# Kernel tuning notes

Measured on AMD Instinct MI355X. Metric: run time of the kernel, lower is better.

Reference implementation:

```python
import jax, jax.numpy as jnp
import numpy as np

B, T = 8, 4096
EMBED_DIM = 128
ENGRAM_EMBED_DIM = 64
VOCAB_SIZES = [4096, 4096]
MAX_NGRAM = 3
NUM_HEADS = 2
N_STREAMS = 4
KERNEL = 4
TOTAL_NGRAMS = len(VOCAB_SIZES) * NUM_HEADS          # 4
INPUT_DIM = TOTAL_NGRAMS * ENGRAM_EMBED_DIM          # 256
TOTAL_SLOTS = sum(VOCAB_SIZES) * NUM_HEADS           # 16384


def setup_inputs() -> dict:
    key = jax.random.key(0)
    ks = jax.random.split(key, 10)
    x = jax.random.normal(ks[0], (B, T, N_STREAMS, EMBED_DIM), dtype=jnp.float32)
    input_ids = jax.random.randint(ks[1], (B, T), 0, 50257, dtype=jnp.int32)
    multipliers = jax.random.randint(ks[2], (MAX_NGRAM - 1, NUM_HEADS, MAX_NGRAM), 1, 10000, dtype=jnp.int32)
    embedding = jax.random.normal(ks[3], (TOTAL_SLOTS, ENGRAM_EMBED_DIM), dtype=jnp.float32) * 0.02
    val_W = jax.random.normal(ks[4], (EMBED_DIM, INPUT_DIM), dtype=jnp.float32) * 0.05
    val_b = jnp.zeros((EMBED_DIM,), jnp.float32)
    key_W = jax.random.normal(ks[5], (N_STREAMS, EMBED_DIM, INPUT_DIM), dtype=jnp.float32) * 0.05
    key_b = jnp.zeros((N_STREAMS, EMBED_DIM), jnp.float32)
    normq_w = jnp.ones((N_STREAMS, EMBED_DIM), jnp.float32)
    normk_w = jnp.ones((N_STREAMS, EMBED_DIM), jnp.float32)
    conv_w = jax.random.normal(ks[6], (N_STREAMS * EMBED_DIM, 1, KERNEL), dtype=jnp.float32) * 0.1
    convnorm_w = jnp.ones((N_STREAMS, EMBED_DIM), jnp.float32)
    return {"x": x, "input_ids": input_ids, "multipliers": multipliers,
            "embedding": embedding, "val_W": val_W, "val_b": val_b,
            "key_W": key_W, "key_b": key_b, "normq_w": normq_w,
            "normk_w": normk_w, "conv_w": conv_w, "convnorm_w": convnorm_w}


def rmsnorm(v, w):
    # torch nn.RMSNorm default eps = finfo(dtype).eps
    eps = jnp.finfo(v.dtype).eps
    return v * jax.lax.rsqrt(jnp.mean(v * v, axis=-1, keepdims=True) + eps) * w


def hash_ids_fn(input_ids, multipliers):
    padded = jnp.pad(input_ids, ((0, 0), (MAX_NGRAM - 1, 0)))            # [B, T+2]
    windows = jnp.stack([padded[:, i:i + T] for i in range(MAX_NGRAM)], axis=-1)  # [B,T,3]
    hashes = []
    for n_idx in range(MAX_NGRAM - 1):
        ngram_len = n_idx + 2
        grams = windows[:, :, MAX_NGRAM - ngram_len:]                    # [B,T,L]
        mults = multipliers[n_idx, :, :ngram_len]                        # [H,L]
        mixed = grams[:, :, None, :] * mults[None, None, :, :]           # [B,T,H,L]
        h = mixed[..., 0]
        for k in range(1, ngram_len):
            h = jnp.bitwise_xor(h, mixed[..., k])
        hashes.append(h % VOCAB_SIZES[n_idx])                            # [B,T,H]
    return jnp.concatenate(hashes, axis=2)                               # [B,T,4]


def engram_forward(x, input_ids, multipliers, embedding, val_W, val_b,
                   key_W, key_b, normq_w, normk_w, conv_w, convnorm_w):
    hids = hash_ids_fn(input_ids, multipliers)
    offsets = jnp.cumsum(jnp.array([0] + [v for v in VOCAB_SIZES for _ in range(NUM_HEADS)], jnp.int32))[:-1]
    ids = hids + offsets                                                 # [B,T,4]
    emb = embedding[ids].reshape(B, T, INPUT_DIM)                        # [B,T,256]
    v_base = emb @ val_W.T + val_b                                       # [B,T,128]
    k = rmsnorm(jnp.einsum('bte,gde->btgd', emb, key_W) + key_b, normk_w)  # [B,T,G,D]
    q = rmsnorm(x, normq_w)                                              # [B,T,G,D]
    score = jnp.sum(q * k, axis=-1, keepdims=True) / (EMBED_DIM ** 0.5)
    gates = jax.nn.sigmoid(score)                                        # [B,T,G,1]
    v_gated = v_base[:, :, None, :] * gates                              # [B,T,G,D]
    # ShortConv: per-chunk RMSNorm -> causal depthwise conv -> SiLU
    xn = rmsnorm(v_gated, convnorm_w).reshape(B, T, N_STREAMS * EMBED_DIM)
    x_bct = jnp.transpose(xn, (0, 2, 1))                                 # [B,C,T]
    x_bct = jnp.pad(x_bct, ((0, 0), (0, 0), (KERNEL - 1, 0)))            # causal left pad
    y_bct = jax.lax.conv_general_dilated(
        x_bct, conv_w, window_strides=(1,), padding='VALID',
        dimension_numbers=('NCH', 'OIH', 'NCH'),
        feature_group_count=N_STREAMS * EMBED_DIM)                       # [B,C,T]
    y = jax.nn.silu(y_bct)
    y = jnp.transpose(y, (0, 2, 1)).reshape(B, T, N_STREAMS, EMBED_DIM)
    return v_gated + y


def reference(x, input_ids, multipliers, embedding, val_W, val_b,
              key_W, key_b, normq_w, normk_w, conv_w, convnorm_w):
    return engram_forward(x, input_ids, multipliers, embedding, val_W, val_b,
                          key_W, key_b, normq_w, normk_w, conv_w, convnorm_w)
```

## Files before the change

### kernel.cpp

```cpp
#include <hip/hip_runtime.h>
#include <math.h>

#define EPS 1.1920928955078125e-07f

typedef __attribute__((ext_vector_type(8)))  short short8;
typedef __attribute__((ext_vector_type(4)))  short short4v;
typedef __attribute__((ext_vector_type(16))) float floatx16;

__device__ __forceinline__ float4 ld4(const float* __restrict__ p) { return *(const float4* __restrict__)p; }
__device__ __forceinline__ void   st4(float* __restrict__ p, float4 v) { *(float4* __restrict__)p = v; }

__device__ __forceinline__ unsigned short f2bf(float f) {
    union { float f; unsigned u; } v; v.f = f;
    unsigned r = v.u + 0x7fffu + ((v.u >> 16) & 1u);
    return (unsigned short)(r >> 16);
}

__global__ __launch_bounds__(256) void build_pack(const float* __restrict__ val_W,
                                                  const float* __restrict__ key_W,
                                                  const float* __restrict__ emb,
                                                  unsigned short* __restrict__ WbF,
                                                  unsigned short* __restrict__ ebf)
{
    int bid = blockIdx.x;
    if (bid < 80) {
        int idx  = bid * 256 + threadIdx.x;
        int lane = idx & 63;
        int ks   = (idx >> 6) & 15;
        int nt   = idx >> 10;
        int n = (nt << 5) + (lane & 31);
        int k = (ks << 4) + ((lane >> 5) << 3);
        const float* src = (n < 512) ? key_W + (size_t)n * 256 + k
                                     : val_W + (size_t)(n - 512) * 256 + k;
        float4 v0 = ld4(src), v1 = ld4(src + 4);
        unsigned short o[8] = { f2bf(v0.x), f2bf(v0.y), f2bf(v0.z), f2bf(v0.w),
                                f2bf(v1.x), f2bf(v1.y), f2bf(v1.z), f2bf(v1.w) };
        unsigned short* dst = WbF + (size_t)idx * 8;
        *(short4v*)dst       = *(short4v*)&o[0];
        *(short4v*)(dst + 4) = *(short4v*)&o[4];
    } else {
        int idx = (bid - 80) * 256 + threadIdx.x;
        const float* src = emb + ((size_t)idx << 3);
        float4 v0 = ld4(src), v1 = ld4(src + 4);
        unsigned short o[8] = { f2bf(v0.x), f2bf(v0.y), f2bf(v0.z), f2bf(v0.w),
                                f2bf(v1.x), f2bf(v1.y), f2bf(v1.z), f2bf(v1.w) };
        unsigned short* dst = ebf + ((size_t)idx << 3);
        *(short4v*)dst       = *(short4v*)&o[0];
        *(short4v*)(dst + 4) = *(short4v*)&o[4];
    }
}

__global__ __launch_bounds__(256, 4) void engram_gemm(
    const float* __restrict__ x,
    const int*   __restrict__ input_ids,
    const int*   __restrict__ mult,
    const unsigned short* __restrict__ ebf,
    const float* __restrict__ val_b,
    const float* __restrict__ key_b,
    const float* __restrict__ normq_w,
    const float* __restrict__ normk_w,
    const unsigned short* __restrict__ WbF,
    float* __restrict__ v_base,
    float* __restrict__ Gbuf,
    float* __restrict__ S2buf)
{
    __shared__ int   sids[32][4];
    __shared__ short A[32 * 260];
    __shared__ float D[32 * 130];

    const int tid  = threadIdx.x;
    const int tok0 = blockIdx.x << 5;

    if (tid < 32) {
        int token = tok0 + tid;
        int b = token >> 12, t = token & 4095;
        const int* row = input_ids + (b << 12);
        unsigned g2 = (unsigned)row[t];
        unsigned g1 = (t >= 1) ? (unsigned)row[t - 1] : 0u;
        unsigned g0 = (t >= 2) ? (unsigned)row[t - 2] : 0u;
        sids[tid][0] = (int)(((g1 * (unsigned)mult[0]) ^ (g2 * (unsigned)mult[1])) & 4095u);
        sids[tid][1] = (int)((((g1 * (unsigned)mult[3]) ^ (g2 * (unsigned)mult[4])) & 4095u) + 4096u);
        sids[tid][2] = (int)((((g0 * (unsigned)mult[6]) ^ (g1 * (unsigned)mult[7]) ^ (g2 * (unsigned)mult[8])) & 4095u) + 8192u);
        sids[tid][3] = (int)((((g0 * (unsigned)mult[9]) ^ (g1 * (unsigned)mult[10]) ^ (g2 * (unsigned)mult[11])) & 4095u) + 12288u);
    }
    __syncthreads();

    #pragma unroll
    for (int it = 0; it < 4; ++it) {
        int f = (it << 8) + tid;
        int token = f >> 5, ch = f & 31;
        const unsigned short* src = ebf + ((size_t)sids[token][ch >> 3] << 6) + ((ch & 7) << 3);
        short4v lo = *(const short4v*)src;
        short4v hi = *(const short4v*)(src + 4);
        short* dst = A + token * 260 + (ch << 3);
        *(short4v*)dst       = lo;
        *(short4v*)(dst + 4) = hi;
    }
    __syncthreads();

    const int lane = tid & 63;
    const int wv   = tid >> 6;
    const int half = lane >> 5;
    const int mrow = lane & 31;

    const short*  Ap = A + mrow * 260 + (half << 3);
    const float4* Bf = (const float4*)WbF + lane;

    const int ty = tid >> 4, tx = tid & 15;
    const int tx8 = tx << 3;
    const int colw = (wv << 5) + mrow;
    const int rb   = half << 2;

    for (int s = 0; s < 4; ++s) {
        const float* xp0 = x + ((((size_t)(tok0 + (ty << 1))     << 2) + s) << 7) + tx8;
        const float* xp1 = x + ((((size_t)(tok0 + (ty << 1) + 1) << 2) + s) << 7) + tx8;
        float4 xa0 = ld4(xp0), xb0 = ld4(xp0 + 4);
        float4 xa1 = ld4(xp1), xb1 = ld4(xp1 + 4);

        floatx16 acc;
        #pragma unroll
        for (int r = 0; r < 16; ++r) acc[r] = 0.f;
        const int nt = (s << 2) + wv;
        const float4* bp = Bf + ((size_t)(nt << 4) << 6);
        #pragma unroll 4
        for (int ks = 0; ks < 16; ++ks) {
            short4v al = *(const short4v*)(Ap + (ks << 4));
            short4v ah = *(const short4v*)(Ap + (ks << 4) + 4);
            short8 a = { al[0], al[1], al[2], al[3], ah[0], ah[1], ah[2], ah[3] };
            union { float4 f; short8 s8; } ub;
            ub.f = bp[(size_t)ks << 6];
            acc = __builtin_amdgcn_mfma_f32_32x32x16_bf16(a, ub.s8, acc, 0, 0, 0);
        }

        __syncthreads();
        #pragma unroll
        for (int r = 0; r < 16; ++r) {
            int row = (r & 3) + ((r >> 2) << 3) + rb;
            D[row * 130 + colw] = acc[r];
        }
        __syncthreads();

        const float* kbp = key_b   + (s << 7) + tx8;
        const float* nqp = normq_w + (s << 7) + tx8;
        const float* nkp = normk_w + (s << 7) + tx8;
        float4 kba = ld4(kbp), kbb = ld4(kbp + 4);
        float4 nqa = ld4(nqp), nqb = ld4(nqp + 4);
        float4 nka = ld4(nkp), nkb = ld4(nkp + 4);
        float kb[8] = {kba.x, kba.y, kba.z, kba.w, kbb.x, kbb.y, kbb.z, kbb.w};
        float nq[8] = {nqa.x, nqa.y, nqa.z, nqa.w, nqb.x, nqb.y, nqb.z, nqb.w};
        float nk[8] = {nka.x, nka.y, nka.z, nka.w, nkb.x, nkb.y, nkb.z, nkb.w};
        #pragma unroll
        for (int jj = 0; jj < 2; ++jj) {
            int t_loc = (ty << 1) + jj;
            int token = tok0 + t_loc;
            const float* dp = D + t_loc * 130 + tx8;
            float kr[8]; float ks2 = 0.f;
            #pragma unroll
            for (int m = 0; m < 8; ++m) { kr[m] = dp[m] + kb[m]; ks2 += kr[m] * kr[m]; }
            float xv[8];
            if (jj == 0) { xv[0]=xa0.x; xv[1]=xa0.y; xv[2]=xa0.z; xv[3]=xa0.w;
                           xv[4]=xb0.x; xv[5]=xb0.y; xv[6]=xb0.z; xv[7]=xb0.w; }
            else         { xv[0]=xa1.x; xv[1]=xa1.y; xv[2]=xa1.z; xv[3]=xa1.w;
                           xv[4]=xb1.x; xv[5]=xb1.y; xv[6]=xb1.z; xv[7]=xb1.w; }
            float xs2 = 0.f, dt = 0.f;
            #pragma unroll
            for (int m = 0; m < 8; ++m) { xs2 += xv[m] * xv[m]; dt += xv[m] * nq[m] * kr[m] * nk[m]; }
            #pragma unroll
            for (int off = 1; off < 16; off <<= 1) {
                ks2 += __shfl_xor(ks2, off);
                xs2 += __shfl_xor(xs2, off);
                dt  += __shfl_xor(dt,  off);
            }
            float sc = dt * rsqrtf(xs2 * (1.f / 128.f) + EPS)
                          * rsqrtf(ks2 * (1.f / 128.f) + EPS) * 0.08838834764831845f;
            float gate = 1.f / (1.f + __expf(-sc));
            if (tx == 0) Gbuf[(token << 2) + s] = gate;
        }
    }

    {
        floatx16 acc;
        #pragma unroll
        for (int r = 0; r < 16; ++r) acc[r] = 0.f;
        const int nt = 16 + wv;
        const float4* bp = Bf + ((size_t)(nt << 4) << 6);
        #pragma unroll 4
        for (int ks = 0; ks < 16; ++ks) {
            short4v al = *(const short4v*)(Ap + (ks << 4));
            short4v ah = *(const short4v*)(Ap + (ks << 4) + 4);
            short8 a = { al[0], al[1], al[2], al[3], ah[0], ah[1], ah[2], ah[3] };
            union { float4 f; short8 s8; } ub;
            ub.f = bp[(size_t)ks << 6];
            acc = __builtin_amdgcn_mfma_f32_32x32x16_bf16(a, ub.s8, acc, 0, 0, 0);
        }
        __syncthreads();
        #pragma unroll
        for (int r = 0; r < 16; ++r) {
            int row = (r & 3) + ((r >> 2) << 3) + rb;
            D[row * 130 + colw] = acc[r];
        }
        __syncthreads();

        const float* vbp = val_b + tx8;
        float4 vba = ld4(vbp), vbb = ld4(vbp + 4);
        float vb[8] = {vba.x, vba.y, vba.z, vba.w, vbb.x, vbb.y, vbb.z, vbb.w};
        #pragma unroll
        for (int jj = 0; jj < 2; ++jj) {
            int t_loc = (ty << 1) + jj;
            int token = tok0 + t_loc;
            const float* dp = D + t_loc * 130 + tx8;
            float v[8]; float s2 = 0.f;
            #pragma unroll
            for (int m = 0; m < 8; ++m) { v[m] = dp[m] + vb[m]; s2 += v[m] * v[m]; }
            #pragma unroll
            for (int off = 1; off < 16; off <<= 1) s2 += __shfl_xor(s2, off);
            float* vp = v_base + ((size_t)token << 7) + tx8;
            st4(vp,     make_float4(v[0], v[1], v[2], v[3]));
            st4(vp + 4, make_float4(v[4], v[5], v[6], v[7]));
            if (tx == 0) S2buf[token] = s2;
        }
    }
}

__global__ __launch_bounds__(256, 4) void engram_out(
    const float* __restrict__ v_base,
    const float* __restrict__ Gbuf,
    const float* __restrict__ S2buf,
    const float* __restrict__ conv_w,
    const float* __restrict__ convnorm_w,
    float* __restrict__ out)
{
    int gid = blockIdx.x * 256 + threadIdx.x;
    int d4  = gid & 31;
    int s   = (gid >> 5) & 3;
    int tok = gid >> 7;
    int seq = tok & 4095;

    float vr[4][4];
    float fw[4];
    float g3 = 0.f;
    #pragma unroll
    for (int k = 0; k < 4; ++k) {
        if (seq + k >= 3) {
            int glob = tok - 3 + k;
            float4 vv = ld4(v_base + ((size_t)glob << 7) + (d4 << 2));
            vr[k][0] = vv.x; vr[k][1] = vv.y; vr[k][2] = vv.z; vr[k][3] = vv.w;
            float gg  = Gbuf[(glob << 2) + s];
            float s2n = S2buf[glob] * (1.f / 128.f);
            fw[k] = gg * rsqrtf(gg * gg * s2n + EPS);
            if (k == 3) g3 = gg;
        } else {
            vr[k][0] = 0.f; vr[k][1] = 0.f; vr[k][2] = 0.f; vr[k][3] = 0.f;
            fw[k] = 0.f;
        }
    }

    const int ch0 = (s << 7) + (d4 << 2);
    float4 cw = ld4(convnorm_w + ch0);
    float  cwn[4] = { cw.x, cw.y, cw.z, cw.w };
    float4 w0 = ld4(conv_w + (size_t)(ch0 + 0) * 4);
    float4 w1 = ld4(conv_w + (size_t)(ch0 + 1) * 4);
    float4 w2 = ld4(conv_w + (size_t)(ch0 + 2) * 4);
    float4 w3 = ld4(conv_w + (size_t)(ch0 + 3) * 4);

    float o[4];
    #pragma unroll
    for (int i = 0; i < 4; ++i) {
        float4 wi = (i == 0) ? w0 : (i == 1) ? w1 : (i == 2) ? w2 : w3;
        float a = wi.x * vr[0][i] * fw[0]
                + wi.y * vr[1][i] * fw[1]
                + wi.z * vr[2][i] * fw[2]
                + wi.w * vr[3][i] * fw[3];
        float y = a * cwn[i];
        o[i] = vr[3][i] * g3 + y / (1.f + __expf(-y));
    }
    st4(out + ((size_t)((tok << 2) + s) << 7) + (d4 << 2),
        make_float4(o[0], o[1], o[2], o[3]));
}

extern "C" void kernel_launch(void* const* d_in, const int* in_sizes, int n_in,
                              void* d_out, int out_size, void* d_ws, size_t ws_size,
                              hipStream_t stream)
{
    const float* x          = (const float*)d_in[0];
    const int*   input_ids  = (const int*)d_in[1];
    const int*   mult       = (const int*)d_in[2];
    const float* embedding  = (const float*)d_in[3];
    const float* val_W      = (const float*)d_in[4];
    const float* val_b      = (const float*)d_in[5];
    const float* key_W      = (const float*)d_in[6];
    const float* key_b      = (const float*)d_in[7];
    const float* normq_w    = (const float*)d_in[8];
    const float* normk_w    = (const float*)d_in[9];
    const float* conv_w     = (const float*)d_in[10];
    const float* convnorm_w = (const float*)d_in[11];
    float* out = (float*)d_out;

    char* ws = (char*)d_ws;
    unsigned short* WbF = (unsigned short*)ws;
    unsigned short* ebf = (unsigned short*)(ws + 327680);
    float* v_base = (float*)(ws + 327680 + 2097152);
    float* Gbuf   = (float*)(ws + 327680 + 2097152 + 16777216);
    float* S2buf  = (float*)(ws + 327680 + 2097152 + 16777216 + 524288);

    build_pack<<<592, 256, 0, stream>>>(val_W, key_W, embedding, WbF, ebf);
    engram_gemm<<<1024, 256, 0, stream>>>(x, input_ids, mult, ebf, val_b, key_b,
                                          normq_w, normk_w, WbF, v_base, Gbuf, S2buf);
    engram_out<<<16384, 256, 0, stream>>>(v_base, Gbuf, S2buf, conv_w, convnorm_w, out);
}
```

Measured before the change: 178.4 us.

## Stage v_base tile in shared memory and slide conv window per thread

The output kernel now assigns 32 tokens per block. It loads the needed 35 rows of v_base plus the per-token norm factors and gates into shared memory once. Each thread then walks 16 consecutive tokens with a register-rotated causal window. This removes the repeated global loads of v_base and the redundant rsqrt computations done for every stream and window position. The grid shrinks sixteenfold and a barrier is added, which reduces available parallelism for latency hiding.

```diff
diff --git a/kernel.cpp b/kernel.cpp
--- a/kernel.cpp
+++ b/kernel.cpp
@@ -230,52 +230,88 @@
     const float* __restrict__ convnorm_w,
     float* __restrict__ out)
 {
-    int gid = blockIdx.x * 256 + threadIdx.x;
-    int d4  = gid & 31;
-    int s   = (gid >> 5) & 3;
-    int tok = gid >> 7;
-    int seq = tok & 4095;
-
-    float vr[4][4];
-    float fw[4];
-    float g3 = 0.f;
-    #pragma unroll
-    for (int k = 0; k < 4; ++k) {
-        if (seq + k >= 3) {
-            int glob = tok - 3 + k;
-            float4 vv = ld4(v_base + ((size_t)glob << 7) + (d4 << 2));
-            vr[k][0] = vv.x; vr[k][1] = vv.y; vr[k][2] = vv.z; vr[k][3] = vv.w;
-            float gg  = Gbuf[(glob << 2) + s];
+    __shared__ float Vs[35 * 128];
+    __shared__ float FWs[35 * 4];
+    __shared__ float Gs[32 * 4];
+
+    const int tid  = threadIdx.x;
+    const int tok0 = blockIdx.x << 5;
+    const int seq0 = tok0 & 4095;
+
+    for (int i = tid; i < 1120; i += 256) {
+        int row = i >> 5;
+        int c4  = i & 31;
+        float4 v;
+        if (seq0 + row >= 3) {
+            int glob = tok0 - 3 + row;
+            v = ld4(v_base + ((size_t)glob << 7) + (c4 << 2));
+        } else {
+            v = make_float4(0.f, 0.f, 0.f, 0.f);
+        }
+        st4(&Vs[row * 128 + (c4 << 2)], v);
+    }
+    if (tid < 140) {
+        int row = tid >> 2;
+        int s   = tid & 3;
+        float fw = 0.f, g = 0.f;
+        if (seq0 + row >= 3) {
+            int glob = tok0 - 3 + row;
+            g = Gbuf[(glob << 2) + s];
             float s2n = S2buf[glob] * (1.f / 128.f);
-            fw[k] = gg * rsqrtf(gg * gg * s2n + EPS);
-            if (k == 3) g3 = gg;
-        } else {
-            vr[k][0] = 0.f; vr[k][1] = 0.f; vr[k][2] = 0.f; vr[k][3] = 0.f;
-            fw[k] = 0.f;
-        }
-    }
+            fw = g * rsqrtf(g * g * s2n + EPS);
+        }
+        FWs[tid] = fw;
+        if (row >= 3) Gs[((row - 3) << 2) + s] = g;
+    }
+    __syncthreads();
+
+    const int d4 = tid & 31;
+    const int s  = (tid >> 5) & 3;
+    const int t0 = (tid >> 7) << 4;
 
     const int ch0 = (s << 7) + (d4 << 2);
-    float4 cw = ld4(convnorm_w + ch0);
-    float  cwn[4] = { cw.x, cw.y, cw.z, cw.w };
+    float4 cwv = ld4(convnorm_w + ch0);
+    float  cwn[4] = { cwv.x, cwv.y, cwv.z, cwv.w };
     float4 w0 = ld4(conv_w + (size_t)(ch0 + 0) * 4);
     float4 w1 = ld4(conv_w + (size_t)(ch0 + 1) * 4);
     float4 w2 = ld4(conv_w + (size_t)(ch0 + 2) * 4);
     float4 w3 = ld4(conv_w + (size_t)(ch0 + 3) * 4);
 
-    float o[4];
+    float vw[4][4];
+    float fwv[4];
     #pragma unroll
-    for (int i = 0; i < 4; ++i) {
-        float4 wi = (i == 0) ? w0 : (i == 1) ? w1 : (i == 2) ? w2 : w3;
-        float a = wi.x * vr[0][i] * fw[0]
-                + wi.y * vr[1][i] * fw[1]
-                + wi.z * vr[2][i] * fw[2]
-                + wi.w * vr[3][i] * fw[3];
-        float y = a * cwn[i];
-        o[i] = vr[3][i] * g3 + y / (1.f + __expf(-y));
-    }
-    st4(out + ((size_t)((tok << 2) + s) << 7) + (d4 << 2),
-        make_float4(o[0], o[1], o[2], o[3]));
+    for (int k = 0; k < 3; ++k) {
+        const float* p = &Vs[(t0 + k) * 128 + (d4 << 2)];
+        vw[k][0] = p[0]; vw[k][1] = p[1]; vw[k][2] = p[2]; vw[k][3] = p[3];
+        fwv[k] = FWs[((t0 + k) << 2) + s];
+    }
+
+    #pragma unroll
+    for (int t = 0; t < 16; ++t) {
+        const int tl = t0 + t;
+        const float* p = &Vs[(tl + 3) * 128 + (d4 << 2)];
+        vw[3][0] = p[0]; vw[3][1] = p[1]; vw[3][2] = p[2]; vw[3][3] = p[3];
+        fwv[3] = FWs[((tl + 3) << 2) + s];
+        const float g3 = Gs[(tl << 2) + s];
+
+        float o[4];
+        #pragma unroll
+        for (int i = 0; i < 4; ++i) {
+            float4 wi = (i == 0) ? w0 : (i == 1) ? w1 : (i == 2) ? w2 : w3;
+            float a = wi.x * vw[0][i] * fwv[0]
+                    + wi.y * vw[1][i] * fwv[1]
+                    + wi.z * vw[2][i] * fwv[2]
+                    + wi.w * vw[3][i] * fwv[3];
+            float y = a * cwn[i];
+            o[i] = vw[3][i] * g3 + y / (1.f + __expf(-y));
+        }
+        st4(out + ((size_t)(((tok0 + tl) << 2) + s) << 7) + (d4 << 2),
+            make_float4(o[0], o[1], o[2], o[3]));
+
+        #pragma unroll
+        for (int i = 0; i < 4; ++i) { vw[0][i] = vw[1][i]; vw[1][i] = vw[2][i]; vw[2][i] = vw[3][i]; }
+        fwv[0] = fwv[1]; fwv[1] = fwv[2]; fwv[2] = fwv[3];
+    }
 }
 
 extern "C" void kernel_launch(void* const* d_in, const int* in_sizes, int n_in,
@@ -306,5 +342,5 @@
     build_pack<<<592, 256, 0, stream>>>(val_W, key_W, embedding, WbF, ebf);
     engram_gemm<<<1024, 256, 0, stream>>>(x, input_ids, mult, ebf, val_b, key_b,
                                           normq_w, normk_w, WbF, v_base, Gbuf, S2buf);
-    engram_out<<<16384, 256, 0, stream>>>(v_base, Gbuf, S2buf, conv_w, convnorm_w, out);
-}
+    engram_out<<<1024, 256, 0, stream>>>(v_base, Gbuf, S2buf, conv_w, convnorm_w, out);
+}
```

Measured after the change: 227.1 us. 1.27x slower.
